# Kernel tuning notes

Measured on AMD Instinct MI355X. Metric: run time of the kernel, lower is better.

The kernel has to match this reference:

```python
import jax, jax.numpy as jnp
import numpy as np

WIN = (9, 9)
EPS = float(np.power(np.e, -15))  # e^-15 threshold from original code


def _box_sum(x, win):
    kernel = jnp.ones((1, 1, win[0], win[1]), dtype=x.dtype)
    p = win[0] // 2
    return jax.lax.conv_general_dilated(
        x, kernel, window_strides=(1, 1), padding=[(p, p), (p, p)],
        dimension_numbers=("NCHW", "OIHW", "NCHW"))


def setup_inputs() -> dict:
    key = jax.random.key(0)
    k1, k2 = jax.random.split(key)
    B, C, H, W = 32, 1, 512, 512
    I = jax.random.normal(k1, (B, C, H, W), dtype=jnp.float32)
    J = jax.random.normal(k2, (B, C, H, W), dtype=jnp.float32)
    return {"I": I, "J": J}


def reference(I, J):
    win = WIN
    win_size = win[0] * win[1]
    I_sum = _box_sum(I, win)
    J_sum = _box_sum(J, win)
    I2_sum = _box_sum(I * I, win)
    J2_sum = _box_sum(J * J, win)
    IJ_sum = _box_sum(I * J, win)

    u_I = I_sum / win_size
    u_J = J_sum / win_size
    cross = IJ_sum - u_J * I_sum - u_I * J_sum + u_I * u_J * win_size
    I_var = I2_sum - 2 * u_I * I_sum + u_I * u_I * win_size
    J_var = J2_sum - 2 * u_J * J_sum + u_J * u_J * win_size

    non_zero = I_var * J_var > EPS
    cross = jnp.where(non_zero, cross, 1.0)
    I_var = jnp.where(non_zero, I_var, 1.0)
    J_var = jnp.where(non_zero, J_var, 1.0)

    cc = cross * cross / (I_var * J_var + EPS)
    return -1.0 * jnp.mean(cc, axis=(1, 2, 3)) + 1.0
```

## Files before the change

kernel.cpp:

```cpp
#include <hip/hip_runtime.h>


#define IMG_H 512
#define IMG_W 512
#define NBATCH 32
#define RPW 32
#define STRIPS_PER_IMG (IMG_H / RPW)
#define RING 11

typedef __attribute__((address_space(3))) void       lds_t;
typedef __attribute__((address_space(1))) const void glob_t;

__global__ __launch_bounds__(64, 1) void lcc_main(const float* __restrict__ I,
                                                  const float* __restrict__ J,
                                                  float* __restrict__ out) {
    __shared__ __align__(16) float ring[RING][1024];

    const int lane  = threadIdx.x;
    const int strip = blockIdx.x;
    const int b  = strip >> 4;
    const int y0 = (strip & 15) * RPW;
    const int x0 = lane * 8;

    const float* __restrict__ Ib = I + (size_t)b * IMG_H * IMG_W;
    const float* __restrict__ Jb = J + (size_t)b * IMG_H * IMG_W;

    auto issue_row = [&](int y) {
        int slot = (y - y0 + 4) % RING;
        const float* gI = Ib + y * IMG_W;
        const float* gJ = Jb + y * IMG_W;
        float* lI = &ring[slot][0];
        float* lJ = &ring[slot][512];
        __builtin_amdgcn_global_load_lds((glob_t*)(gI +       lane * 4), (lds_t*)lI,         16, 0, 0);
        __builtin_amdgcn_global_load_lds((glob_t*)(gI + 256 + lane * 4), (lds_t*)(lI + 256), 16, 0, 0);
        __builtin_amdgcn_global_load_lds((glob_t*)(gJ +       lane * 4), (lds_t*)lJ,         16, 0, 0);
        __builtin_amdgcn_global_load_lds((glob_t*)(gJ + 256 + lane * 4), (lds_t*)(lJ + 256), 16, 0, 0);
    };

    float sI[8]  = {0.f,0.f,0.f,0.f,0.f,0.f,0.f,0.f};
    float sJ[8]  = {0.f,0.f,0.f,0.f,0.f,0.f,0.f,0.f};
    float sII[8] = {0.f,0.f,0.f,0.f,0.f,0.f,0.f,0.f};
    float sJJ[8] = {0.f,0.f,0.f,0.f,0.f,0.f,0.f,0.f};
    float sIJ[8] = {0.f,0.f,0.f,0.f,0.f,0.f,0.f,0.f};

    auto add_ld = [&](int y) {
        int slot = (y - y0 + 4) % RING;
        const float4* pI = reinterpret_cast<const float4*>(&ring[slot][x0]);
        const float4* pJ = reinterpret_cast<const float4*>(&ring[slot][512 + x0]);
        float4 i0 = pI[0], i1 = pI[1], j0 = pJ[0], j1 = pJ[1];
        float iv[8] = {i0.x,i0.y,i0.z,i0.w,i1.x,i1.y,i1.z,i1.w};
        float jv[8] = {j0.x,j0.y,j0.z,j0.w,j1.x,j1.y,j1.z,j1.w};
        #pragma unroll
        for (int c = 0; c < 8; ++c) {
            sI[c]  += iv[c];
            sJ[c]  += jv[c];
            sII[c]  = fmaf(iv[c], iv[c], sII[c]);
            sJJ[c]  = fmaf(jv[c], jv[c], sJJ[c]);
            sIJ[c]  = fmaf(iv[c], jv[c], sIJ[c]);
        }
    };
    auto sub_ld = [&](int y) {
        int slot = (y - y0 + 4) % RING;
        const float4* pI = reinterpret_cast<const float4*>(&ring[slot][x0]);
        const float4* pJ = reinterpret_cast<const float4*>(&ring[slot][512 + x0]);
        float4 i0 = pI[0], i1 = pI[1], j0 = pJ[0], j1 = pJ[1];
        float iv[8] = {i0.x,i0.y,i0.z,i0.w,i1.x,i1.y,i1.z,i1.w};
        float jv[8] = {j0.x,j0.y,j0.z,j0.w,j1.x,j1.y,j1.z,j1.w};
        #pragma unroll
        for (int c = 0; c < 8; ++c) {
            sI[c]  -= iv[c];
            sJ[c]  -= jv[c];
            sII[c]  = fmaf(-iv[c], iv[c], sII[c]);
            sJJ[c]  = fmaf(-jv[c], jv[c], sJJ[c]);
            sIJ[c]  = fmaf(-iv[c], jv[c], sIJ[c]);
        }
    };

    auto hsum = [&](const float (&s)[8], float (&h)[8]) {
        float w[16];
        #pragma unroll
        for (int c = 0; c < 8; ++c) w[4+c] = s[c];
        #pragma unroll
        for (int c = 0; c < 4; ++c) {
            float a = __shfl_up(s[4+c], 1);
            w[c] = lane ? a : 0.f;
            a = __shfl_down(s[c], 1);
            w[12+c] = (lane < 63) ? a : 0.f;
        }
        float acc = 0.f;
        #pragma unroll
        for (int i = 0; i < 9; ++i) acc += w[i];
        h[0] = acc;
        #pragma unroll
        for (int k = 1; k < 8; ++k) { acc += w[k+8] - w[k-1]; h[k] = acc; }
    };

    const int wy_lo = (y0 - 4 < 0) ? 0 : y0 - 4;
    const int wy_hi = y0 + 4;
    #pragma unroll 1
    for (int y = wy_lo; y <= wy_hi; ++y) issue_row(y);
    issue_row(y0 + 5);
    __builtin_amdgcn_s_waitcnt(0x3F74);
    #pragma unroll 1
    for (int y = wy_lo; y <= wy_hi; ++y) add_ld(y);

    const float inv81 = 1.0f / 81.0f;
    const float EPSV  = 3.0590232050182579e-07f;
    float local = 0.0f;

    #pragma unroll 1
    for (int r = 0; r < RPW; ++r) {
        const int t = y0 + r;

        const bool issued_next = (r + 2 < RPW) && (t + 6 < IMG_H);
        if (issued_next) {
            __builtin_amdgcn_s_waitcnt(0xC07F);
            issue_row(t + 6);
        }

        float hI[8], hJ[8], hII[8], hJJ[8], hIJ[8];
        hsum(sI,  hI);
        hsum(sJ,  hJ);
        hsum(sII, hII);
        hsum(sJJ, hJJ);
        hsum(sIJ, hIJ);

        #pragma unroll
        for (int k = 0; k < 8; ++k) {
            float cross = fmaf(hI[k] * hJ[k], -inv81, hIJ[k]);
            float Iv    = fmaf(hI[k] * hI[k], -inv81, hII[k]);
            float Jv    = fmaf(hJ[k] * hJ[k], -inv81, hJJ[k]);
            float p  = Iv * Jv;
            bool  nz = p > EPSV;
            float c2 = nz ? cross : 1.0f;
            float p2 = nz ? p : 1.0f;
            local += (c2 * c2) * __builtin_amdgcn_rcpf(p2 + EPSV);
        }

        if (r + 1 < RPW) {
            if (issued_next) __builtin_amdgcn_s_waitcnt(0x3F74);
            else             __builtin_amdgcn_s_waitcnt(0x3F70);
            if (t + 5 < IMG_H) add_ld(t + 5);
            if (t - 4 >= 0)    sub_ld(t - 4);
        }
    }

    #pragma unroll
    for (int off = 32; off > 0; off >>= 1) local += __shfl_down(local, off);
    if (lane == 0)
        atomicAdd(out + b, fmaf(local, -1.0f / (float)(IMG_H * IMG_W),
                                1.0f / (float)STRIPS_PER_IMG));
}

extern "C" void kernel_launch(void* const* d_in, const int* in_sizes, int n_in,
                              void* d_out, int out_size, void* d_ws, size_t ws_size,
                              hipStream_t stream) {
    const float* I = (const float*)d_in[0];
    const float* J = (const float*)d_in[1];
    float* out = (float*)d_out;

    const int total_strips = NBATCH * STRIPS_PER_IMG;
    lcc_main<<<total_strips, 64, 0, stream>>>(I, J, out);
}
```

Before: 119.1 us.

## Split each row strip across four waves with LDS halo exchange

Each block now runs four waves instead of one. Each wave owns a 128-column segment and each lane handles 2 columns instead of 8, which cuts per-thread register state and raises parallelism from 512 single-wave blocks to 2048 waves. The horizontal 9-tap sum now uses shuffles, plus a double-buffered LDS halo array to pass boundary sums between neighbouring waves. This adds one block-wide barrier per row and more shuffles per output pixel.

```diff
diff --git a/kernel.cpp b/kernel.cpp
--- a/kernel.cpp
+++ b/kernel.cpp
@@ -7,102 +7,68 @@
 #define RPW 32
 #define STRIPS_PER_IMG (IMG_H / RPW)
 #define RING 11
+#define WAVES 4
 
 typedef __attribute__((address_space(3))) void       lds_t;
 typedef __attribute__((address_space(1))) const void glob_t;
 
-__global__ __launch_bounds__(64, 1) void lcc_main(const float* __restrict__ I,
-                                                  const float* __restrict__ J,
-                                                  float* __restrict__ out) {
-    __shared__ __align__(16) float ring[RING][1024];
+__global__ __launch_bounds__(256, 2) void lcc_main(const float* __restrict__ I,
+                                                   const float* __restrict__ J,
+                                                   float* __restrict__ out) {
+    __shared__ __align__(16) float ring[RING * 1024];
+    __shared__ __align__(16) float halo[2][2][WAVES][5][4];
 
-    const int lane  = threadIdx.x;
-    const int strip = blockIdx.x;
-    const int b  = strip >> 4;
-    const int y0 = (strip & 15) * RPW;
-    const int x0 = lane * 8;
+    const int tid  = threadIdx.x;
+    const int lane = tid & 63;
+    const int w    = tid >> 6;
+    const int b  = blockIdx.x >> 4;
+    const int y0 = (blockIdx.x & 15) * RPW;
+    const int seg = w * 128;
 
-    const float* __restrict__ Ib = I + (size_t)b * IMG_H * IMG_W;
-    const float* __restrict__ Jb = J + (size_t)b * IMG_H * IMG_W;
+    const float* __restrict__ Ib = I + (size_t)b * (IMG_H * IMG_W);
+    const float* __restrict__ Jb = J + (size_t)b * (IMG_H * IMG_W);
 
     auto issue_row = [&](int y) {
         int slot = (y - y0 + 4) % RING;
-        const float* gI = Ib + y * IMG_W;
-        const float* gJ = Jb + y * IMG_W;
-        float* lI = &ring[slot][0];
-        float* lJ = &ring[slot][512];
-        __builtin_amdgcn_global_load_lds((glob_t*)(gI +       lane * 4), (lds_t*)lI,         16, 0, 0);
-        __builtin_amdgcn_global_load_lds((glob_t*)(gI + 256 + lane * 4), (lds_t*)(lI + 256), 16, 0, 0);
-        __builtin_amdgcn_global_load_lds((glob_t*)(gJ +       lane * 4), (lds_t*)lJ,         16, 0, 0);
-        __builtin_amdgcn_global_load_lds((glob_t*)(gJ + 256 + lane * 4), (lds_t*)(lJ + 256), 16, 0, 0);
+        const float* src = (lane < 32)
+            ? (Ib + y * IMG_W + seg + lane * 4)
+            : (Jb + y * IMG_W + seg + (lane - 32) * 4);
+        __builtin_amdgcn_global_load_lds((glob_t*)src,
+            (lds_t*)&ring[slot * 1024 + w * 256], 16, 0, 0);
     };
 
-    float sI[8]  = {0.f,0.f,0.f,0.f,0.f,0.f,0.f,0.f};
-    float sJ[8]  = {0.f,0.f,0.f,0.f,0.f,0.f,0.f,0.f};
-    float sII[8] = {0.f,0.f,0.f,0.f,0.f,0.f,0.f,0.f};
-    float sJJ[8] = {0.f,0.f,0.f,0.f,0.f,0.f,0.f,0.f};
-    float sIJ[8] = {0.f,0.f,0.f,0.f,0.f,0.f,0.f,0.f};
+    float s0[5] = {0,0,0,0,0}, s1[5] = {0,0,0,0,0};
 
     auto add_ld = [&](int y) {
         int slot = (y - y0 + 4) % RING;
-        const float4* pI = reinterpret_cast<const float4*>(&ring[slot][x0]);
-        const float4* pJ = reinterpret_cast<const float4*>(&ring[slot][512 + x0]);
-        float4 i0 = pI[0], i1 = pI[1], j0 = pJ[0], j1 = pJ[1];
-        float iv[8] = {i0.x,i0.y,i0.z,i0.w,i1.x,i1.y,i1.z,i1.w};
-        float jv[8] = {j0.x,j0.y,j0.z,j0.w,j1.x,j1.y,j1.z,j1.w};
-        #pragma unroll
-        for (int c = 0; c < 8; ++c) {
-            sI[c]  += iv[c];
-            sJ[c]  += jv[c];
-            sII[c]  = fmaf(iv[c], iv[c], sII[c]);
-            sJJ[c]  = fmaf(jv[c], jv[c], sJJ[c]);
-            sIJ[c]  = fmaf(iv[c], jv[c], sIJ[c]);
-        }
+        const float* sb = &ring[slot * 1024 + w * 256];
+        float2 iv = *reinterpret_cast<const float2*>(&sb[2 * lane]);
+        float2 jv = *reinterpret_cast<const float2*>(&sb[128 + 2 * lane]);
+        s0[0] += iv.x;                        s1[0] += iv.y;
+        s0[1] += jv.x;                        s1[1] += jv.y;
+        s0[2] = fmaf(iv.x, iv.x, s0[2]);      s1[2] = fmaf(iv.y, iv.y, s1[2]);
+        s0[3] = fmaf(jv.x, jv.x, s0[3]);      s1[3] = fmaf(jv.y, jv.y, s1[3]);
+        s0[4] = fmaf(iv.x, jv.x, s0[4]);      s1[4] = fmaf(iv.y, jv.y, s1[4]);
     };
     auto sub_ld = [&](int y) {
         int slot = (y - y0 + 4) % RING;
-        const float4* pI = reinterpret_cast<const float4*>(&ring[slot][x0]);
-        const float4* pJ = reinterpret_cast<const float4*>(&ring[slot][512 + x0]);
-        float4 i0 = pI[0], i1 = pI[1], j0 = pJ[0], j1 = pJ[1];
-        float iv[8] = {i0.x,i0.y,i0.z,i0.w,i1.x,i1.y,i1.z,i1.w};
-        float jv[8] = {j0.x,j0.y,j0.z,j0.w,j1.x,j1.y,j1.z,j1.w};
-        #pragma unroll
-        for (int c = 0; c < 8; ++c) {
-            sI[c]  -= iv[c];
-            sJ[c]  -= jv[c];
-            sII[c]  = fmaf(-iv[c], iv[c], sII[c]);
-            sJJ[c]  = fmaf(-jv[c], jv[c], sJJ[c]);
-            sIJ[c]  = fmaf(-iv[c], jv[c], sIJ[c]);
-        }
-    };
-
-    auto hsum = [&](const float (&s)[8], float (&h)[8]) {
-        float w[16];
-        #pragma unroll
-        for (int c = 0; c < 8; ++c) w[4+c] = s[c];
-        #pragma unroll
-        for (int c = 0; c < 4; ++c) {
-            float a = __shfl_up(s[4+c], 1);
-            w[c] = lane ? a : 0.f;
-            a = __shfl_down(s[c], 1);
-            w[12+c] = (lane < 63) ? a : 0.f;
-        }
-        float acc = 0.f;
-        #pragma unroll
-        for (int i = 0; i < 9; ++i) acc += w[i];
-        h[0] = acc;
-        #pragma unroll
-        for (int k = 1; k < 8; ++k) { acc += w[k+8] - w[k-1]; h[k] = acc; }
+        const float* sb = &ring[slot * 1024 + w * 256];
+        float2 iv = *reinterpret_cast<const float2*>(&sb[2 * lane]);
+        float2 jv = *reinterpret_cast<const float2*>(&sb[128 + 2 * lane]);
+        s0[0] -= iv.x;                        s1[0] -= iv.y;
+        s0[1] -= jv.x;                        s1[1] -= jv.y;
+        s0[2] = fmaf(-iv.x, iv.x, s0[2]);     s1[2] = fmaf(-iv.y, iv.y, s1[2]);
+        s0[3] = fmaf(-jv.x, jv.x, s0[3]);     s1[3] = fmaf(-jv.y, jv.y, s1[3]);
+        s0[4] = fmaf(-iv.x, jv.x, s0[4]);     s1[4] = fmaf(-iv.y, jv.y, s1[4]);
     };
 
     const int wy_lo = (y0 - 4 < 0) ? 0 : y0 - 4;
-    const int wy_hi = y0 + 4;
     #pragma unroll 1
-    for (int y = wy_lo; y <= wy_hi; ++y) issue_row(y);
+    for (int y = wy_lo; y <= y0 + 4; ++y) issue_row(y);
     issue_row(y0 + 5);
-    __builtin_amdgcn_s_waitcnt(0x3F74);
+    asm volatile("s_waitcnt vmcnt(1)" ::: "memory");
     #pragma unroll 1
-    for (int y = wy_lo; y <= wy_hi; ++y) add_ld(y);
+    for (int y = wy_lo; y <= y0 + 4; ++y) add_ld(y);
 
     const float inv81 = 1.0f / 81.0f;
     const float EPSV  = 3.0590232050182579e-07f;
@@ -110,26 +76,69 @@
 
     #pragma unroll 1
     for (int r = 0; r < RPW; ++r) {
-        const int t = y0 + r;
+        const int t   = y0 + r;
+        const int buf = r & 1;
 
-        const bool issued_next = (r + 2 < RPW) && (t + 6 < IMG_H);
-        if (issued_next) {
-            __builtin_amdgcn_s_waitcnt(0xC07F);
-            issue_row(t + 6);
+        if (lane < 2) {
+            #pragma unroll
+            for (int q = 0; q < 5; ++q) {
+                halo[buf][0][w][q][2 * lane]     = s0[q];
+                halo[buf][0][w][q][2 * lane + 1] = s1[q];
+            }
+        }
+        if (lane >= 62) {
+            int o = 2 * (lane - 62);
+            #pragma unroll
+            for (int q = 0; q < 5; ++q) {
+                halo[buf][1][w][q][o]     = s0[q];
+                halo[buf][1][w][q][o + 1] = s1[q];
+            }
         }
 
-        float hI[8], hJ[8], hII[8], hJJ[8], hIJ[8];
-        hsum(sI,  hI);
-        hsum(sJ,  hJ);
-        hsum(sII, hII);
-        hsum(sJJ, hJJ);
-        hsum(sIJ, hIJ);
+        const bool issued = (r <= RPW - 3) && (t + 6 < IMG_H);
+        if (issued) issue_row(t + 6);
 
+        asm volatile("s_waitcnt lgkmcnt(0)\n\ts_barrier" ::: "memory");
+
+        float h0[5], h1[5];
         #pragma unroll
-        for (int k = 0; k < 8; ++k) {
-            float cross = fmaf(hI[k] * hJ[k], -inv81, hIJ[k]);
-            float Iv    = fmaf(hI[k] * hI[k], -inv81, hII[k]);
-            float Jv    = fmaf(hJ[k] * hJ[k], -inv81, hJJ[k]);
+        for (int q = 0; q < 5; ++q) {
+            float a0 = s0[q], a1 = s1[q];
+            float u2_0 = __shfl_up(a0, 2),   u2_1 = __shfl_up(a1, 2);
+            float u1_0 = __shfl_up(a0, 1),   u1_1 = __shfl_up(a1, 1);
+            float d1_0 = __shfl_down(a0, 1), d1_1 = __shfl_down(a1, 1);
+            float d2_0 = __shfl_down(a0, 2), d2_1 = __shfl_down(a1, 2);
+            if (lane < 2) {
+                float4 hR = make_float4(0.f, 0.f, 0.f, 0.f);
+                if (w > 0) hR = *reinterpret_cast<const float4*>(&halo[buf][1][w - 1][q][0]);
+                if (lane == 0) { u2_0 = hR.x; u2_1 = hR.y; u1_0 = hR.z; u1_1 = hR.w; }
+                else           { u2_0 = hR.z; u2_1 = hR.w; }
+            }
+            if (lane >= 62) {
+                float4 hL = make_float4(0.f, 0.f, 0.f, 0.f);
+                if (w < 3) hL = *reinterpret_cast<const float4*>(&halo[buf][0][w + 1][q][0]);
+                if (lane == 63) { d1_0 = hL.x; d1_1 = hL.y; d2_0 = hL.z; d2_1 = hL.w; }
+                else            { d2_0 = hL.x; d2_1 = hL.y; }
+            }
+            float t9 = u2_0 + u2_1 + u1_0 + u1_1 + a0 + a1 + d1_0 + d1_1 + d2_0;
+            h0[q] = t9;
+            h1[q] = t9 - u2_0 + d2_1;
+        }
+
+        {
+            float cross = fmaf(h0[0] * h0[1], -inv81, h0[4]);
+            float Iv    = fmaf(h0[0] * h0[0], -inv81, h0[2]);
+            float Jv    = fmaf(h0[1] * h0[1], -inv81, h0[3]);
+            float p  = Iv * Jv;
+            bool  nz = p > EPSV;
+            float c2 = nz ? cross : 1.0f;
+            float p2 = nz ? p : 1.0f;
+            local += (c2 * c2) * __builtin_amdgcn_rcpf(p2 + EPSV);
+        }
+        {
+            float cross = fmaf(h1[0] * h1[1], -inv81, h1[4]);
+            float Iv    = fmaf(h1[0] * h1[0], -inv81, h1[2]);
+            float Jv    = fmaf(h1[1] * h1[1], -inv81, h1[3]);
             float p  = Iv * Jv;
             bool  nz = p > EPSV;
             float c2 = nz ? cross : 1.0f;
@@ -138,10 +147,13 @@
         }
 
         if (r + 1 < RPW) {
-            if (issued_next) __builtin_amdgcn_s_waitcnt(0x3F74);
-            else             __builtin_amdgcn_s_waitcnt(0x3F70);
-            if (t + 5 < IMG_H) add_ld(t + 5);
-            if (t - 4 >= 0)    sub_ld(t - 4);
+            int ya = t + 5, yr = t - 4;
+            if (ya < IMG_H) {
+                if (issued) asm volatile("s_waitcnt vmcnt(1)" ::: "memory");
+                else        asm volatile("s_waitcnt vmcnt(0)" ::: "memory");
+                add_ld(ya);
+            }
+            if (yr >= 0) sub_ld(yr);
         }
     }
 
@@ -149,7 +161,7 @@
     for (int off = 32; off > 0; off >>= 1) local += __shfl_down(local, off);
     if (lane == 0)
         atomicAdd(out + b, fmaf(local, -1.0f / (float)(IMG_H * IMG_W),
-                                1.0f / (float)STRIPS_PER_IMG));
+                                1.0f / (float)(STRIPS_PER_IMG * WAVES)));
 }
 
 extern "C" void kernel_launch(void* const* d_in, const int* in_sizes, int n_in,
@@ -159,6 +171,6 @@
     const float* J = (const float*)d_in[1];
     float* out = (float*)d_out;
 
-    const int total_strips = NBATCH * STRIPS_PER_IMG;
-    lcc_main<<<total_strips, 64, 0, stream>>>(I, J, out);
+    const int total_blocks = NBATCH * STRIPS_PER_IMG;
+    lcc_main<<<total_blocks, 256, 0, stream>>>(I, J, out);
 }
```

Measured after the change: 154.8 us. +30.0%, slower.
